# Kernel tuning notes

Measured on AMD Instinct MI355X. Metric: run time of the kernel, lower is better.

The kernel has to match this reference:

```python
import jax, jax.numpy as jnp
import numpy as np

B, S, L, H, N_ITEMS = 16, 20, 64, 768, 50000  # sessions, max items/session, tokens/item, hidden, catalog
T = S * L
TEMP = 0.05       # config.temp
PAD_POS = 50      # pad item position id (see torch code)
EPS = 1e-8        # torch CosineSimilarity eps


def setup_inputs() -> dict:
    key = jax.random.key(0)
    k1, k2, k3, k4 = jax.random.split(key, 4)
    hidden = jax.random.normal(k1, (B, T, H), jnp.float32)
    emb = jax.random.normal(k2, (N_ITEMS, H), jnp.float32)
    # item position ids: each item's L tokens share position 1..S; padded items -> 50
    pos = np.tile(np.repeat(np.arange(1, S + 1), L)[None, :], (B, 1))  # [B,T]
    sess_len = np.asarray(jax.random.randint(k3, (B,), S // 2, S + 1))  # items per session
    item_idx = np.repeat(np.arange(S), L)[None, :]                      # [1,T]
    pos = np.where(item_idx < sess_len[:, None], pos, PAD_POS).astype(np.int32)
    attn = (pos != PAD_POS).astype(np.int32)
    attrs = np.asarray(jax.random.randint(k4, (B, T), 0, 4)).astype(np.int32)
    return {
        "hidden_states": hidden,
        "item_embedding": emb,
        "attention_mask": jnp.asarray(attn),
        "item_position_ids": jnp.asarray(pos),
        "attr_type_ids": jnp.asarray(attrs),
    }


def reference(hidden_states, item_embedding, attention_mask, item_position_ids, attr_type_ids):
    # --- RecformerPooler (pooler_type='item'): nan-mean pool tokens per item ---
    item_ids = jnp.arange(1, S + 1, dtype=item_position_ids.dtype)
    mask = item_position_ids[:, None, :] == item_ids[None, :, None]      # [B,S,T]
    counts = mask.sum(-1)                                                # [B,S]
    valid = counts > 0                                                   # items present in session
    maskf = mask.astype(hidden_states.dtype)
    pooled = jnp.einsum('bst,bth->bsh', maskf, hidden_states)
    pooled = pooled / jnp.maximum(counts, 1)[..., None].astype(hidden_states.dtype)
    # (torch produces NaN rows for invalid items; we carry `valid` instead)

    # --- Similarity: cosine / temp vs full item catalog ---
    pn = jnp.maximum(jnp.linalg.norm(pooled, axis=-1, keepdims=True), EPS)
    en = jnp.maximum(jnp.linalg.norm(item_embedding, axis=-1, keepdims=True), EPS)
    sim = jnp.einsum('bsh,nh->bns', pooled / pn, item_embedding / en) / TEMP  # [B,N,S]

    # --- reduce_session('maxsim'): NaN -> -inf, max over session items ---
    sim = jnp.where(valid[:, None, :], sim, -jnp.inf)
    scores = sim.max(axis=-1)  # [B, N]; trailing mean over attr dim (size 1) is identity
    return scores
```

## Files before the change

### kernel.cpp

```cpp
#include <hip/hip_runtime.h>

#define B_ 16
#define S_ 20
#define L_ 64
#define T_ 1280
#define H_ 768
#define NITEMS 50000
#define TEMP 0.05f
#define EPSN 1e-8f

#define BM 320
#define BN 64
#define BK 32
#define NKT (H_ / BK)

typedef __attribute__((ext_vector_type(8))) short short8;
typedef __attribute__((ext_vector_type(4))) short short4v;
typedef __attribute__((ext_vector_type(4))) float f32x4;

__device__ __forceinline__ unsigned short f2bf(float f) {
    unsigned int u = __float_as_uint(f);
    u = u + 0x7FFFu + ((u >> 16) & 1u);
    return (unsigned short)(u >> 16);
}

typedef __attribute__((address_space(3))) void lds_void;
typedef const __attribute__((address_space(1))) void gbl_void;
__device__ __forceinline__ void load_lds16(const void* g, void* l) {
    __builtin_amdgcn_global_load_lds((gbl_void*)g, (lds_void*)l, 16, 0, 0);
}

__global__ __launch_bounds__(384) void pool_kernel(const float* __restrict__ hidden,
                                                   const int* __restrict__ pos,
                                                   unsigned short* __restrict__ A,
                                                   int* __restrict__ valid) {
    const int row = blockIdx.x;
    const int b = row / S_, s = row % S_;
    const int tid = threadIdx.x;

    __shared__ float wgt[L_];
    __shared__ int cntS;
    __shared__ float red[6];

    const int* pbase = pos + b * T_ + s * L_;
    if (tid < L_) {
        const int match = (pbase[tid] == s + 1) ? 1 : 0;
        unsigned long long bal = __ballot(match);
        wgt[tid] = match ? 1.0f : 0.0f;
        if (tid == 0) cntS = (int)__popcll(bal);
    }
    __syncthreads();

    const int cnt = cntS;
    const float inv = 1.0f / (float)(cnt > 0 ? cnt : 1);
    const float* hbase = hidden + ((size_t)b * T_ + (size_t)s * L_) * H_ + tid * 2;

    float a0 = 0.f, a1 = 0.f;
#pragma unroll 8
    for (int t = 0; t < L_; ++t) {
        const float w = wgt[t];
        const float2 v = *reinterpret_cast<const float2*>(hbase + (size_t)t * H_);
        a0 += w * v.x; a1 += w * v.y;
    }
    a0 *= inv; a1 *= inv;

    float ss = a0 * a0 + a1 * a1;
#pragma unroll
    for (int off = 32; off; off >>= 1) ss += __shfl_xor(ss, off, 64);
    const int wave = tid >> 6, lane = tid & 63;
    if (lane == 0) red[wave] = ss;
    __syncthreads();
    const float tot = red[0] + red[1] + red[2] + red[3] + red[4] + red[5];
    const float scale = 1.0f / (fmaxf(sqrtf(tot), EPSN) * TEMP);

    const int chunk = tid >> 4;
    const int cSlot = (tid >> 2) & 3;
    const int phys = cSlot ^ ((row >> 1) & 3);
    unsigned short r0 = f2bf(a0 * scale);
    unsigned short r1 = f2bf(a1 * scale);
    unsigned int pk = (unsigned int)r0 | ((unsigned int)r1 << 16);
    *reinterpret_cast<unsigned int*>(A + (size_t)row * H_ + chunk * 32 + phys * 8 +
                                     ((tid * 2) & 7)) = pk;
    if (tid == 0) valid[row] = (cnt > 0) ? 1 : 0;
}

__global__ __launch_bounds__(256, 3) void gemm_kernel(const float* __restrict__ emb,
                                                      const unsigned short* __restrict__ A,
                                                      const int* __restrict__ valid,
                                                      float* __restrict__ out) {
    const int n0 = blockIdx.x * BN;
    const int tid = threadIdx.x;
    const int wave = tid >> 6, lane = tid & 63, quad = lane >> 4, lq = lane & 15;

    __shared__ alignas(16) short As[2][BM * BK];
    __shared__ alignas(16) short Bs[2][BN * BK];
    __shared__ float sEn[BN];
    __shared__ int sMask[B_];

    if (tid < B_) {
        int m = 0;
        for (int s = 0; s < S_; ++s) m |= (valid[tid * S_ + s] ? 1 : 0) << s;
        sMask[tid] = m;
    }

    const unsigned short* aSrc = A + (size_t)(tid >> 2) * H_ + (tid & 3) * 8;
    const int brLoc = tid >> 2;
    int brGlb = n0 + brLoc;
    if (brGlb > NITEMS - 1) brGlb = NITEMS - 1;
    const float* bSrc = emb + (size_t)brGlb * H_ + (tid & 3) * 8;
    const int bw = brLoc * BK + (((tid & 3) ^ ((brLoc >> 1) & 3)) * 8);

    float rowSq = 0.f;

    {
        const float4 v0 = *reinterpret_cast<const float4*>(bSrc);
        const float4 v1 = *reinterpret_cast<const float4*>(bSrc + 4);
#pragma unroll
        for (int i = 0; i < 5; ++i)
            load_lds16(aSrc + i * 64 * H_, (char*)(&As[0][0]) + tid * 16 + i * 4096);
        rowSq += v0.x * v0.x + v0.y * v0.y + v0.z * v0.z + v0.w * v0.w;
        rowSq += v1.x * v1.x + v1.y * v1.y + v1.z * v1.z + v1.w * v1.w;
        short8 pk;
        pk[0] = (short)f2bf(v0.x); pk[1] = (short)f2bf(v0.y);
        pk[2] = (short)f2bf(v0.z); pk[3] = (short)f2bf(v0.w);
        pk[4] = (short)f2bf(v1.x); pk[5] = (short)f2bf(v1.y);
        pk[6] = (short)f2bf(v1.z); pk[7] = (short)f2bf(v1.w);
        *reinterpret_cast<short8*>(&Bs[0][bw]) = pk;
    }
    asm volatile("s_waitcnt vmcnt(0)" ::: "memory");
    __syncthreads();

    f32x4 acc[5][4];
#pragma unroll
    for (int i = 0; i < 5; ++i)
#pragma unroll
        for (int j = 0; j < 4; ++j) acc[i][j] = (f32x4)0.f;

    const int fswz = (lq >> 1) & 3;
    int cur = 0;
    for (int kt = 0; kt < NKT; ++kt) {
        const bool more = (kt + 1 < NKT);
        float4 v0, v1;
        if (more) {
            const int k0 = (kt + 1) * BK;
            v0 = *reinterpret_cast<const float4*>(bSrc + k0);
            v1 = *reinterpret_cast<const float4*>(bSrc + k0 + 4);
        }
        if (more) asm volatile("s_waitcnt vmcnt(2)" ::: "memory");
        else      asm volatile("s_waitcnt vmcnt(0)" ::: "memory");
        __builtin_amdgcn_s_barrier();
        __builtin_amdgcn_sched_barrier(0);
        asm volatile("" ::: "memory");
        if (more) {
            const int k0 = (kt + 1) * BK;
#pragma unroll
            for (int i = 0; i < 5; ++i)
                load_lds16(aSrc + k0 + i * 64 * H_,
                           (char*)(&As[cur ^ 1][0]) + tid * 16 + i * 4096);
        }
        short8 bF[4];
#pragma unroll
        for (int nf = 0; nf < 4; ++nf) {
            const int rB = nf * 16 + lq;
            bF[nf] = *reinterpret_cast<const short8*>(
                &Bs[cur][rB * BK + ((quad ^ fswz) * 8)]);
        }
        __builtin_amdgcn_s_setprio(1);
#pragma unroll
        for (int mf = 0; mf < 5; ++mf) {
            const int rA = wave * 80 + mf * 16 + lq;
            const short8 aF = *reinterpret_cast<const short8*>(
                &As[cur][rA * BK + ((quad ^ fswz) * 8)]);
#pragma unroll
            for (int nf = 0; nf < 4; ++nf)
                acc[mf][nf] =
                    __builtin_amdgcn_mfma_f32_16x16x32_bf16(aF, bF[nf], acc[mf][nf], 0, 0, 0);
        }
        __builtin_amdgcn_s_setprio(0);
        if (more) {
            rowSq += v0.x * v0.x + v0.y * v0.y + v0.z * v0.z + v0.w * v0.w;
            rowSq += v1.x * v1.x + v1.y * v1.y + v1.z * v1.z + v1.w * v1.w;
            short8 pk;
            pk[0] = (short)f2bf(v0.x); pk[1] = (short)f2bf(v0.y);
            pk[2] = (short)f2bf(v0.z); pk[3] = (short)f2bf(v0.w);
            pk[4] = (short)f2bf(v1.x); pk[5] = (short)f2bf(v1.y);
            pk[6] = (short)f2bf(v1.z); pk[7] = (short)f2bf(v1.w);
            *reinterpret_cast<short8*>(&Bs[cur ^ 1][bw]) = pk;
        }
        asm volatile("s_waitcnt lgkmcnt(0)" ::: "memory");
        cur ^= 1;
    }

    rowSq += __shfl_xor(rowSq, 1, 64);
    rowSq += __shfl_xor(rowSq, 2, 64);
    if (!(tid & 3)) sEn[brLoc] = fmaxf(sqrtf(rowSq), EPSN);
    __syncthreads();

#pragma unroll
    for (int nf = 0; nf < 4; ++nf) {
        const int ncol = nf * 16 + lq;
        const int n = n0 + ncol;
        const float inv_en = 1.0f / sEn[ncol];
#pragma unroll
        for (int bl = 0; bl < 4; ++bl) {
            const int bb = wave * 4 + bl;
            const int msk = sMask[bb];
            const int rLo = bl * S_;
            float lm = -__builtin_inff();
            const int mfLo = rLo >> 4;
            const int mfHi = (rLo + S_ - 1) >> 4;
#pragma unroll
            for (int mf = mfLo; mf <= mfHi; ++mf)
#pragma unroll
                for (int e = 0; e < 4; ++e) {
                    const int r = mf * 16 + quad * 4 + e;
                    const unsigned off = (unsigned)(r - rLo);
                    const bool ok = (off < (unsigned)S_) && ((msk >> off) & 1);
                    lm = ok ? fmaxf(lm, acc[mf][nf][e]) : lm;
                }
            lm = fmaxf(lm, __shfl_xor(lm, 16, 64));
            lm = fmaxf(lm, __shfl_xor(lm, 32, 64));
            if (quad == 0 && n < NITEMS)
                out[(size_t)bb * NITEMS + n] = lm * inv_en;
        }
    }
}

extern "C" void kernel_launch(void* const* d_in, const int* in_sizes, int n_in,
                              void* d_out, int out_size, void* d_ws, size_t ws_size,
                              hipStream_t stream) {
    const float* hidden = (const float*)d_in[0];
    const float* emb    = (const float*)d_in[1];
    const int*   pos    = (const int*)d_in[3];
    float* out = (float*)d_out;

    unsigned short* Abf = (unsigned short*)d_ws;
    int* valid = (int*)((char*)d_ws + (size_t)320 * 768 * 2);

    pool_kernel<<<dim3(320), dim3(384), 0, stream>>>(hidden, pos, Abf, valid);
    gemm_kernel<<<dim3((NITEMS + BN - 1) / BN), dim3(256), 0, stream>>>(emb, Abf, valid, out);
}
```

Baseline: 314.1 us.

## Split GEMM into single-wave blocks with XCD-aware mapping and direct fp32 LDS loads

The GEMM kernel is restructured so that each 64-thread block computes 80 pooled rows (4 sessions) against 64 catalog items, replacing the 256-thread block that covered all 320 rows. The grid is remapped so the four row-slices of one item chunk land on the same XCD, which lets them share the embedding rows in L2. Embedding rows are now streamed as fp32 straight into LDS with async global_load_lds, and are converted to bf16 and squared for the norm at fragment-read time. Single-wave blocks need no barriers, and the grid exposes more parallelism. In exchange, each embedding tile is converted and its norm computed four times, and global or L2 traffic for the embedding rises.

Measured after the change: 343.0 us. +9.2%, slower.

```diff
diff --git a/kernel.cpp b/kernel.cpp
--- a/kernel.cpp
+++ b/kernel.cpp
@@ -9,13 +9,15 @@
 #define TEMP 0.05f
 #define EPSN 1e-8f
 
-#define BM 320
-#define BN 64
 #define BK 32
 #define NKT (H_ / BK)
+#define BM1 80
+#define BN1 64
+#define NCHUNK 782
+#define PERX 98
+#define GRID1 (8 * 4 * PERX)
 
 typedef __attribute__((ext_vector_type(8))) short short8;
-typedef __attribute__((ext_vector_type(4))) short short4v;
 typedef __attribute__((ext_vector_type(4))) float f32x4;
 
 __device__ __forceinline__ unsigned short f2bf(float f) {
@@ -84,127 +86,117 @@
     if (tid == 0) valid[row] = (cnt > 0) ? 1 : 0;
 }
 
-__global__ __launch_bounds__(256, 3) void gemm_kernel(const float* __restrict__ emb,
-                                                      const unsigned short* __restrict__ A,
-                                                      const int* __restrict__ valid,
-                                                      float* __restrict__ out) {
-    const int n0 = blockIdx.x * BN;
-    const int tid = threadIdx.x;
-    const int wave = tid >> 6, lane = tid & 63, quad = lane >> 4, lq = lane & 15;
-
-    __shared__ alignas(16) short As[2][BM * BK];
-    __shared__ alignas(16) short Bs[2][BN * BK];
-    __shared__ float sEn[BN];
-    __shared__ int sMask[B_];
-
-    if (tid < B_) {
-        int m = 0;
-        for (int s = 0; s < S_; ++s) m |= (valid[tid * S_ + s] ? 1 : 0) << s;
-        sMask[tid] = m;
-    }
-
-    const unsigned short* aSrc = A + (size_t)(tid >> 2) * H_ + (tid & 3) * 8;
-    const int brLoc = tid >> 2;
-    int brGlb = n0 + brLoc;
-    if (brGlb > NITEMS - 1) brGlb = NITEMS - 1;
-    const float* bSrc = emb + (size_t)brGlb * H_ + (tid & 3) * 8;
-    const int bw = brLoc * BK + (((tid & 3) ^ ((brLoc >> 1) & 3)) * 8);
-
-    float rowSq = 0.f;
-
-    {
-        const float4 v0 = *reinterpret_cast<const float4*>(bSrc);
-        const float4 v1 = *reinterpret_cast<const float4*>(bSrc + 4);
-#pragma unroll
-        for (int i = 0; i < 5; ++i)
-            load_lds16(aSrc + i * 64 * H_, (char*)(&As[0][0]) + tid * 16 + i * 4096);
-        rowSq += v0.x * v0.x + v0.y * v0.y + v0.z * v0.z + v0.w * v0.w;
-        rowSq += v1.x * v1.x + v1.y * v1.y + v1.z * v1.z + v1.w * v1.w;
-        short8 pk;
-        pk[0] = (short)f2bf(v0.x); pk[1] = (short)f2bf(v0.y);
-        pk[2] = (short)f2bf(v0.z); pk[3] = (short)f2bf(v0.w);
-        pk[4] = (short)f2bf(v1.x); pk[5] = (short)f2bf(v1.y);
-        pk[6] = (short)f2bf(v1.z); pk[7] = (short)f2bf(v1.w);
-        *reinterpret_cast<short8*>(&Bs[0][bw]) = pk;
-    }
-    asm volatile("s_waitcnt vmcnt(0)" ::: "memory");
-    __syncthreads();
+__global__ __launch_bounds__(64) void gemm_kernel(const float* __restrict__ emb,
+                                                  const unsigned short* __restrict__ A,
+                                                  const int* __restrict__ valid,
+                                                  float* __restrict__ out) {
+    const int i = blockIdx.x;
+    const int xcd = i & 7;
+    const int k = i >> 3;
+    const int m = k & 3;
+    const int nc = xcd * PERX + (k >> 2);
+    if (nc >= NCHUNK) return;
+    const int n0 = nc * BN1;
+
+    const int lane = threadIdx.x;
+    const int quad = lane >> 4, lq = lane & 15;
+
+    __shared__ alignas(16) short As[2][BM1 * BK];
+    __shared__ alignas(16) float Bs[2][BN1 * BK];
+    __shared__ int sMask[4];
+
+    if (lane < 4) {
+        int mm = 0;
+        for (int s = 0; s < S_; ++s) mm |= (valid[(m * 4 + lane) * S_ + s] ? 1 : 0) << s;
+        sMask[lane] = mm;
+    }
+
+    const unsigned short* aSrc = A + (size_t)(m * BM1 + (lane >> 2)) * H_ + (lane & 3) * 8;
+    const int bCol = (((lane & 7) ^ (lane >> 3)) * 4);
+    const float* bPtr[8];
+#pragma unroll
+    for (int i1 = 0; i1 < 8; ++i1) {
+        int r = n0 + i1 * 8 + (lane >> 3);
+        if (r > NITEMS - 1) r = NITEMS - 1;
+        bPtr[i1] = emb + (size_t)r * H_ + bCol;
+    }
+
+#define STAGE(bufidx, k0)                                                              \
+    do {                                                                               \
+        _Pragma("unroll") for (int i0 = 0; i0 < 5; ++i0)                               \
+            load_lds16(aSrc + (k0) + i0 * 16 * H_,                                     \
+                       (char*)(&As[bufidx][0]) + lane * 16 + i0 * 1024);               \
+        _Pragma("unroll") for (int i1 = 0; i1 < 8; ++i1)                               \
+            load_lds16(bPtr[i1] + (k0), (char*)(&Bs[bufidx][0]) + lane * 16 + i1 * 1024); \
+    } while (0)
+
+    STAGE(0, 0);
 
     f32x4 acc[5][4];
 #pragma unroll
-    for (int i = 0; i < 5; ++i)
-#pragma unroll
-        for (int j = 0; j < 4; ++j) acc[i][j] = (f32x4)0.f;
-
-    const int fswz = (lq >> 1) & 3;
-    int cur = 0;
+    for (int a = 0; a < 5; ++a)
+#pragma unroll
+        for (int b = 0; b < 4; ++b) acc[a][b] = (f32x4)0.f;
+    float enAcc[4] = {0.f, 0.f, 0.f, 0.f};
+
+    const int fswzA = (lq >> 1) & 3;
+    const int swzB = lq & 7;
+
     for (int kt = 0; kt < NKT; ++kt) {
-        const bool more = (kt + 1 < NKT);
-        float4 v0, v1;
-        if (more) {
+        const int buf = kt & 1;
+        if (kt + 1 < NKT) {
             const int k0 = (kt + 1) * BK;
-            v0 = *reinterpret_cast<const float4*>(bSrc + k0);
-            v1 = *reinterpret_cast<const float4*>(bSrc + k0 + 4);
-        }
-        if (more) asm volatile("s_waitcnt vmcnt(2)" ::: "memory");
-        else      asm volatile("s_waitcnt vmcnt(0)" ::: "memory");
-        __builtin_amdgcn_s_barrier();
-        __builtin_amdgcn_sched_barrier(0);
-        asm volatile("" ::: "memory");
-        if (more) {
-            const int k0 = (kt + 1) * BK;
-#pragma unroll
-            for (int i = 0; i < 5; ++i)
-                load_lds16(aSrc + k0 + i * 64 * H_,
-                           (char*)(&As[cur ^ 1][0]) + tid * 16 + i * 4096);
-        }
+            STAGE(buf ^ 1, k0);
+            asm volatile("s_waitcnt vmcnt(13)" ::: "memory");
+        } else {
+            asm volatile("s_waitcnt vmcnt(0)" ::: "memory");
+        }
+
         short8 bF[4];
 #pragma unroll
         for (int nf = 0; nf < 4; ++nf) {
-            const int rB = nf * 16 + lq;
-            bF[nf] = *reinterpret_cast<const short8*>(
-                &Bs[cur][rB * BK + ((quad ^ fswz) * 8)]);
-        }
-        __builtin_amdgcn_s_setprio(1);
+            const int r = nf * 16 + lq;
+            const f32x4 x = *reinterpret_cast<const f32x4*>(
+                &Bs[buf][r * BK + (((quad * 2) ^ swzB) * 4)]);
+            const f32x4 y = *reinterpret_cast<const f32x4*>(
+                &Bs[buf][r * BK + (((quad * 2 + 1) ^ swzB) * 4)]);
+            enAcc[nf] += x[0] * x[0] + x[1] * x[1] + x[2] * x[2] + x[3] * x[3] +
+                         y[0] * y[0] + y[1] * y[1] + y[2] * y[2] + y[3] * y[3];
+            short8 f;
+            f[0] = (short)f2bf(x[0]); f[1] = (short)f2bf(x[1]);
+            f[2] = (short)f2bf(x[2]); f[3] = (short)f2bf(x[3]);
+            f[4] = (short)f2bf(y[0]); f[5] = (short)f2bf(y[1]);
+            f[6] = (short)f2bf(y[2]); f[7] = (short)f2bf(y[3]);
+            bF[nf] = f;
+        }
+
 #pragma unroll
         for (int mf = 0; mf < 5; ++mf) {
-            const int rA = wave * 80 + mf * 16 + lq;
             const short8 aF = *reinterpret_cast<const short8*>(
-                &As[cur][rA * BK + ((quad ^ fswz) * 8)]);
+                &As[buf][(mf * 16 + lq) * BK + ((quad ^ fswzA) * 8)]);
 #pragma unroll
             for (int nf = 0; nf < 4; ++nf)
                 acc[mf][nf] =
                     __builtin_amdgcn_mfma_f32_16x16x32_bf16(aF, bF[nf], acc[mf][nf], 0, 0, 0);
         }
-        __builtin_amdgcn_s_setprio(0);
-        if (more) {
-            rowSq += v0.x * v0.x + v0.y * v0.y + v0.z * v0.z + v0.w * v0.w;
-            rowSq += v1.x * v1.x + v1.y * v1.y + v1.z * v1.z + v1.w * v1.w;
-            short8 pk;
-            pk[0] = (short)f2bf(v0.x); pk[1] = (short)f2bf(v0.y);
-            pk[2] = (short)f2bf(v0.z); pk[3] = (short)f2bf(v0.w);
-            pk[4] = (short)f2bf(v1.x); pk[5] = (short)f2bf(v1.y);
-            pk[6] = (short)f2bf(v1.z); pk[7] = (short)f2bf(v1.w);
-            *reinterpret_cast<short8*>(&Bs[cur ^ 1][bw]) = pk;
-        }
-        asm volatile("s_waitcnt lgkmcnt(0)" ::: "memory");
-        cur ^= 1;
-    }
-
-    rowSq += __shfl_xor(rowSq, 1, 64);
-    rowSq += __shfl_xor(rowSq, 2, 64);
-    if (!(tid & 3)) sEn[brLoc] = fmaxf(sqrtf(rowSq), EPSN);
-    __syncthreads();
-
+    }
+#undef STAGE
+
+    float inv_en[4];
 #pragma unroll
     for (int nf = 0; nf < 4; ++nf) {
-        const int ncol = nf * 16 + lq;
-        const int n = n0 + ncol;
-        const float inv_en = 1.0f / sEn[ncol];
+        float e = enAcc[nf];
+        e += __shfl_xor(e, 16, 64);
+        e += __shfl_xor(e, 32, 64);
+        inv_en[nf] = 1.0f / fmaxf(sqrtf(e), EPSN);
+    }
+
+#pragma unroll
+    for (int nf = 0; nf < 4; ++nf) {
+        const int n = n0 + nf * 16 + lq;
 #pragma unroll
         for (int bl = 0; bl < 4; ++bl) {
-            const int bb = wave * 4 + bl;
-            const int msk = sMask[bb];
+            const int msk = sMask[bl];
             const int rLo = bl * S_;
             float lm = -__builtin_inff();
             const int mfLo = rLo >> 4;
@@ -221,7 +213,7 @@
             lm = fmaxf(lm, __shfl_xor(lm, 16, 64));
             lm = fmaxf(lm, __shfl_xor(lm, 32, 64));
             if (quad == 0 && n < NITEMS)
-                out[(size_t)bb * NITEMS + n] = lm * inv_en;
+                out[(size_t)(m * 4 + bl) * NITEMS + n] = lm * inv_en[nf];
         }
     }
 }
@@ -238,5 +230,5 @@
     int* valid = (int*)((char*)d_ws + (size_t)320 * 768 * 2);
 
     pool_kernel<<<dim3(320), dim3(384), 0, stream>>>(hidden, pos, Abf, valid);
-    gemm_kernel<<<dim3((NITEMS + BN - 1) / BN), dim3(256), 0, stream>>>(emb, Abf, valid, out);
-}
+    gemm_kernel<<<dim3(GRID1), dim3(64), 0, stream>>>(emb, Abf, valid, out);
+}
```

## Stage full-K embedding tile in LDS and stream pooled A from global/L2

Applied to the files above, without the earlier changes.

The GEMM kernel now loads a whole 32-row slice of the item embedding (all 768 columns) into LDS up front, converting it to bf16 and computing row norms in one pass. The pooled A matrix is read straight from global memory (L2-resident) into registers with a two-stage software prefetch, so the per-k-tile LDS staging and barriers for A are gone. Block width drops from 64 to 32 items, which doubles the grid and the number of times the A reads are repeated. The pool kernel writes A in plain row-major order instead of the swizzled layout. Risks include heavy L2 traffic for A, more total A reads, and an upfront load phase with no overlap against compute.

Result: slower. 350.0 us (+11.4%).

```diff
diff --git a/kernel.cpp b/kernel.cpp
--- a/kernel.cpp
+++ b/kernel.cpp
@@ -9,13 +9,11 @@
 #define TEMP 0.05f
 #define EPSN 1e-8f
 
-#define BM 320
-#define BN 64
-#define BK 32
-#define NKT (H_ / BK)
+#define BN2 32
+#define NKT 24
+#define NCHUNK ((NITEMS + BN2 - 1) / BN2)
 
 typedef __attribute__((ext_vector_type(8))) short short8;
-typedef __attribute__((ext_vector_type(4))) short short4v;
 typedef __attribute__((ext_vector_type(4))) float f32x4;
 
 __device__ __forceinline__ unsigned short f2bf(float f) {
@@ -23,11 +21,8 @@
     u = u + 0x7FFFu + ((u >> 16) & 1u);
     return (unsigned short)(u >> 16);
 }
-
-typedef __attribute__((address_space(3))) void lds_void;
-typedef const __attribute__((address_space(1))) void gbl_void;
-__device__ __forceinline__ void load_lds16(const void* g, void* l) {
-    __builtin_amdgcn_global_load_lds((gbl_void*)g, (lds_void*)l, 16, 0, 0);
+__device__ __forceinline__ unsigned int pack2bf(float a, float b) {
+    return (unsigned int)f2bf(a) | ((unsigned int)f2bf(b) << 16);
 }
 
 __global__ __launch_bounds__(384) void pool_kernel(const float* __restrict__ hidden,
@@ -73,14 +68,8 @@
     const float tot = red[0] + red[1] + red[2] + red[3] + red[4] + red[5];
     const float scale = 1.0f / (fmaxf(sqrtf(tot), EPSN) * TEMP);
 
-    const int chunk = tid >> 4;
-    const int cSlot = (tid >> 2) & 3;
-    const int phys = cSlot ^ ((row >> 1) & 3);
-    unsigned short r0 = f2bf(a0 * scale);
-    unsigned short r1 = f2bf(a1 * scale);
-    unsigned int pk = (unsigned int)r0 | ((unsigned int)r1 << 16);
-    *reinterpret_cast<unsigned int*>(A + (size_t)row * H_ + chunk * 32 + phys * 8 +
-                                     ((tid * 2) & 7)) = pk;
+    *reinterpret_cast<unsigned int*>(A + (size_t)row * H_ + tid * 2) =
+        pack2bf(a0 * scale, a1 * scale);
     if (tid == 0) valid[row] = (cnt > 0) ? 1 : 0;
 }
 
@@ -88,13 +77,12 @@
                                                       const unsigned short* __restrict__ A,
                                                       const int* __restrict__ valid,
                                                       float* __restrict__ out) {
-    const int n0 = blockIdx.x * BN;
+    const int n0 = blockIdx.x * BN2;
     const int tid = threadIdx.x;
     const int wave = tid >> 6, lane = tid & 63, quad = lane >> 4, lq = lane & 15;
 
-    __shared__ alignas(16) short As[2][BM * BK];
-    __shared__ alignas(16) short Bs[2][BN * BK];
-    __shared__ float sEn[BN];
+    __shared__ alignas(16) short Bs[BN2 * H_];
+    __shared__ float sEn[BN2];
     __shared__ int sMask[B_];
 
     if (tid < B_) {
@@ -103,101 +91,92 @@
         sMask[tid] = m;
     }
 
-    const unsigned short* aSrc = A + (size_t)(tid >> 2) * H_ + (tid & 3) * 8;
-    const int brLoc = tid >> 2;
-    int brGlb = n0 + brLoc;
-    if (brGlb > NITEMS - 1) brGlb = NITEMS - 1;
-    const float* bSrc = emb + (size_t)brGlb * H_ + (tid & 3) * 8;
-    const int bw = brLoc * BK + (((tid & 3) ^ ((brLoc >> 1) & 3)) * 8);
-
-    float rowSq = 0.f;
-
     {
-        const float4 v0 = *reinterpret_cast<const float4*>(bSrc);
-        const float4 v1 = *reinterpret_cast<const float4*>(bSrc + 4);
-#pragma unroll
-        for (int i = 0; i < 5; ++i)
-            load_lds16(aSrc + i * 64 * H_, (char*)(&As[0][0]) + tid * 16 + i * 4096);
-        rowSq += v0.x * v0.x + v0.y * v0.y + v0.z * v0.z + v0.w * v0.w;
-        rowSq += v1.x * v1.x + v1.y * v1.y + v1.z * v1.z + v1.w * v1.w;
-        short8 pk;
-        pk[0] = (short)f2bf(v0.x); pk[1] = (short)f2bf(v0.y);
-        pk[2] = (short)f2bf(v0.z); pk[3] = (short)f2bf(v0.w);
-        pk[4] = (short)f2bf(v1.x); pk[5] = (short)f2bf(v1.y);
-        pk[6] = (short)f2bf(v1.z); pk[7] = (short)f2bf(v1.w);
-        *reinterpret_cast<short8*>(&Bs[0][bw]) = pk;
-    }
-    asm volatile("s_waitcnt vmcnt(0)" ::: "memory");
+        const int lrB = wave * 8;
+        const float* src[8];
+#pragma unroll
+        for (int rr = 0; rr < 8; ++rr) {
+            int gr = n0 + lrB + rr;
+            if (gr > NITEMS - 1) gr = NITEMS - 1;
+            src[rr] = emb + (size_t)gr * H_ + lane * 4;
+        }
+        f32x4 v[8][3];
+#pragma unroll
+        for (int rr = 0; rr < 8; ++rr)
+#pragma unroll
+            for (int s = 0; s < 3; ++s)
+                v[rr][s] = *reinterpret_cast<const f32x4*>(src[rr] + s * 256);
+#pragma unroll
+        for (int rr = 0; rr < 8; ++rr) {
+            const int r = lrB + rr;
+            float ss = 0.f;
+#pragma unroll
+            for (int s = 0; s < 3; ++s)
+                ss += v[rr][s][0] * v[rr][s][0] + v[rr][s][1] * v[rr][s][1] +
+                      v[rr][s][2] * v[rr][s][2] + v[rr][s][3] * v[rr][s][3];
+#pragma unroll
+            for (int off = 32; off; off >>= 1) ss += __shfl_xor(ss, off, 64);
+            if (lane == 0) sEn[r] = fmaxf(sqrtf(ss), EPSN);
+#pragma unroll
+            for (int s = 0; s < 3; ++s) {
+                const int slot = s * 32 + (lane >> 1);
+                const int phys = (slot & ~7) | ((slot & 7) ^ (r & 7));
+                unsigned int p0 = pack2bf(v[rr][s][0], v[rr][s][1]);
+                unsigned int p1 = pack2bf(v[rr][s][2], v[rr][s][3]);
+                uint2* dst = reinterpret_cast<uint2*>(
+                    (char*)(&Bs[0]) + r * (H_ * 2) + phys * 16 + (lane & 1) * 8);
+                *dst = make_uint2(p0, p1);
+            }
+        }
+    }
     __syncthreads();
 
-    f32x4 acc[5][4];
-#pragma unroll
-    for (int i = 0; i < 5; ++i)
-#pragma unroll
-        for (int j = 0; j < 4; ++j) acc[i][j] = (f32x4)0.f;
-
-    const int fswz = (lq >> 1) & 3;
-    int cur = 0;
-    for (int kt = 0; kt < NKT; ++kt) {
-        const bool more = (kt + 1 < NKT);
-        float4 v0, v1;
-        if (more) {
-            const int k0 = (kt + 1) * BK;
-            v0 = *reinterpret_cast<const float4*>(bSrc + k0);
-            v1 = *reinterpret_cast<const float4*>(bSrc + k0 + 4);
-        }
-        if (more) asm volatile("s_waitcnt vmcnt(2)" ::: "memory");
-        else      asm volatile("s_waitcnt vmcnt(0)" ::: "memory");
-        __builtin_amdgcn_s_barrier();
-        __builtin_amdgcn_sched_barrier(0);
-        asm volatile("" ::: "memory");
-        if (more) {
-            const int k0 = (kt + 1) * BK;
-#pragma unroll
-            for (int i = 0; i < 5; ++i)
-                load_lds16(aSrc + k0 + i * 64 * H_,
-                           (char*)(&As[cur ^ 1][0]) + tid * 16 + i * 4096);
-        }
-        short8 bF[4];
-#pragma unroll
-        for (int nf = 0; nf < 4; ++nf) {
-            const int rB = nf * 16 + lq;
-            bF[nf] = *reinterpret_cast<const short8*>(
-                &Bs[cur][rB * BK + ((quad ^ fswz) * 8)]);
-        }
-        __builtin_amdgcn_s_setprio(1);
-#pragma unroll
-        for (int mf = 0; mf < 5; ++mf) {
-            const int rA = wave * 80 + mf * 16 + lq;
-            const short8 aF = *reinterpret_cast<const short8*>(
-                &As[cur][rA * BK + ((quad ^ fswz) * 8)]);
-#pragma unroll
-            for (int nf = 0; nf < 4; ++nf)
-                acc[mf][nf] =
-                    __builtin_amdgcn_mfma_f32_16x16x32_bf16(aF, bF[nf], acc[mf][nf], 0, 0, 0);
-        }
-        __builtin_amdgcn_s_setprio(0);
-        if (more) {
-            rowSq += v0.x * v0.x + v0.y * v0.y + v0.z * v0.z + v0.w * v0.w;
-            rowSq += v1.x * v1.x + v1.y * v1.y + v1.z * v1.z + v1.w * v1.w;
-            short8 pk;
-            pk[0] = (short)f2bf(v0.x); pk[1] = (short)f2bf(v0.y);
-            pk[2] = (short)f2bf(v0.z); pk[3] = (short)f2bf(v0.w);
-            pk[4] = (short)f2bf(v1.x); pk[5] = (short)f2bf(v1.y);
-            pk[6] = (short)f2bf(v1.z); pk[7] = (short)f2bf(v1.w);
-            *reinterpret_cast<short8*>(&Bs[cur ^ 1][bw]) = pk;
-        }
-        asm volatile("s_waitcnt lgkmcnt(0)" ::: "memory");
-        cur ^= 1;
-    }
-
-    rowSq += __shfl_xor(rowSq, 1, 64);
-    rowSq += __shfl_xor(rowSq, 2, 64);
-    if (!(tid & 3)) sEn[brLoc] = fmaxf(sqrtf(rowSq), EPSN);
-    __syncthreads();
-
-#pragma unroll
-    for (int nf = 0; nf < 4; ++nf) {
+    f32x4 acc[5][2];
+#pragma unroll
+    for (int a = 0; a < 5; ++a)
+#pragma unroll
+        for (int b = 0; b < 2; ++b) acc[a][b] = (f32x4)0.f;
+
+    const unsigned short* aBase[5];
+#pragma unroll
+    for (int mf = 0; mf < 5; ++mf)
+        aBase[mf] = A + (size_t)(wave * 80 + mf * 16 + lq) * H_ + quad * 8;
+
+#define LOADA(dst, kt)                                                           \
+    _Pragma("unroll") for (int mf = 0; mf < 5; ++mf)                             \
+        dst[mf] = *reinterpret_cast<const short8*>(aBase[mf] + (kt) * 32)
+
+#define BREAD(dst, kt)                                                           \
+    _Pragma("unroll") for (int nf = 0; nf < 2; ++nf) {                           \
+        const int r_ = nf * 16 + lq;                                             \
+        const int slot_ = (kt) * 4 + quad;                                       \
+        const int phys_ = (slot_ & ~7) | ((slot_ & 7) ^ (lq & 7));               \
+        dst[nf] = *reinterpret_cast<const short8*>((const char*)(&Bs[0]) +       \
+                                                   r_ * (H_ * 2) + phys_ * 16);  \
+    }
+
+#define MFMAS(af, bf)                                                            \
+    _Pragma("unroll") for (int mf = 0; mf < 5; ++mf)                             \
+        _Pragma("unroll") for (int nf = 0; nf < 2; ++nf)                         \
+            acc[mf][nf] = __builtin_amdgcn_mfma_f32_16x16x32_bf16(               \
+                af[mf], bf[nf], acc[mf][nf], 0, 0, 0)
+
+    short8 aA[5], aB[5], bA[2], bB[2];
+    LOADA(aA, 0);
+    for (int kt = 0; kt < NKT; kt += 2) {
+        LOADA(aB, kt + 1);
+        BREAD(bA, kt);
+        MFMAS(aA, bA);
+        if (kt + 2 < NKT) LOADA(aA, kt + 2);
+        BREAD(bB, kt + 1);
+        MFMAS(aB, bB);
+    }
+#undef LOADA
+#undef BREAD
+#undef MFMAS
+
+#pragma unroll
+    for (int nf = 0; nf < 2; ++nf) {
         const int ncol = nf * 16 + lq;
         const int n = n0 + ncol;
         const float inv_en = 1.0f / sEn[ncol];
@@ -238,5 +217,5 @@
     int* valid = (int*)((char*)d_ws + (size_t)320 * 768 * 2);
 
     pool_kernel<<<dim3(320), dim3(384), 0, stream>>>(hidden, pos, Abf, valid);
-    gemm_kernel<<<dim3((NITEMS + BN - 1) / BN), dim3(256), 0, stream>>>(emb, Abf, valid, out);
-}
+    gemm_kernel<<<dim3(NCHUNK), dim3(256), 0, stream>>>(emb, Abf, valid, out);
+}
```
